# Kernel optimization log

Measured on AMD Instinct MI355X. Metric: run time of the kernel, lower is better.

Reference implementation:

```python
import jax, jax.numpy as jnp
import numpy as np
import math

B, L = 4, 4096
D_MODEL = 1024
D_INNER = 1024          # expand=1
D_STATE = 1             # required by rearrange 'b d 1 l' in ssm()
D_CONV = 2
DT_RANK = 64            # ceil(1024/16)
EPS = 1e-5


def setup_inputs() -> dict:
    key = jax.random.key(0)
    ks = jax.random.split(key, 8)
    dt_min, dt_max, dt_floor = 1e-3, 1e-1, 1e-4
    # dt_proj bias init: inverse-softplus of log-uniform dt (faithful to dt_init)
    dt = jnp.exp(jax.random.uniform(ks[5], (D_INNER,)) * (math.log(dt_max) - math.log(dt_min)) + math.log(dt_min))
    dt = jnp.clip(dt, dt_floor, None)
    inv_dt = dt + jnp.log(-jnp.expm1(-dt))
    std = DT_RANK ** -0.5
    return {
        "x": jax.random.normal(ks[0], (B, L, D_MODEL), dtype=jnp.float32),
        "w_in": jax.random.normal(ks[1], (2 * D_INNER, D_MODEL), dtype=jnp.float32) * 0.02,
        "conv_w": jax.random.normal(ks[2], (D_INNER, 1, D_CONV), dtype=jnp.float32) * 0.5,
        "conv_b": jnp.zeros((D_INNER,), dtype=jnp.float32),
        "x_proj_weight": jax.random.normal(ks[3], (DT_RANK + 2 * D_STATE, D_INNER), dtype=jnp.float32) * 0.02,
        "dt_projs_weight": jax.random.uniform(ks[4], (D_INNER, DT_RANK), minval=-std, maxval=std, dtype=jnp.float32),
        "dt_projs_bias": inv_dt,
        "A_logs": jnp.tile(jnp.log(jnp.arange(1, D_STATE + 1, dtype=jnp.float32))[None, :], (D_INNER, 1)),
        "Ds": jnp.ones((D_INNER,), dtype=jnp.float32),
        "ln_w": jnp.ones((D_INNER,), dtype=jnp.float32),
        "ln_b": jnp.zeros((D_INNER,), dtype=jnp.float32),
        "w_out": jax.random.normal(ks[6], (D_MODEL, D_INNER), dtype=jnp.float32) * 0.02,
    }


def _selective_scan(u, delta, A, Bs):
    # u, delta: (B, D, L); A: (D, N); Bs: (B, N, L) -> hidden states h: (B, D, N, L)
    dA = jnp.exp(jnp.einsum('bdl,dn->bdnl', delta, A))            # (B,D,N,L)
    dBu = jnp.einsum('bdl,bnl,bdl->bdnl', delta, Bs, u)           # delta * B * u
    dA_t = jnp.moveaxis(dA, -1, 0)                                # (L,B,D,N)
    dBu_t = jnp.moveaxis(dBu, -1, 0)

    def step(h, inp):
        a_t, bu_t = inp
        h = a_t * h + bu_t
        return h, h

    h0 = jnp.zeros(dA.shape[:-1], dtype=u.dtype)
    _, hs = jax.lax.scan(step, h0, (dA_t, dBu_t))                 # (L,B,D,N)
    return jnp.moveaxis(hs, 0, -1)                                # (B,D,N,L)


def reference(x, w_in, conv_w, conv_b, x_proj_weight, dt_projs_weight,
              dt_projs_bias, A_logs, Ds, ln_w, ln_b, w_out):
    Bsz, Lsz, _ = x.shape
    # in_proj (bias=False), chunk into x and gate z
    xz = x @ w_in.T                                               # (B,L,2*D)
    xc, z = xz[..., :D_INNER], xz[..., D_INNER:]
    xc = jnp.transpose(xc, (0, 2, 1))                             # (B,D,L)
    # depthwise causal conv1d, padding=d_conv-1, truncated to L
    xc = jax.lax.conv_general_dilated(
        xc, conv_w, window_strides=(1,), padding=[(D_CONV - 1, D_CONV - 1)],
        feature_group_count=D_INNER,
        dimension_numbers=('NCH', 'OIH', 'NCH'))[..., :Lsz]
    xc = xc + conv_b[None, :, None]
    xc = jax.nn.silu(xc)
    # ssm()
    x_dbl = jnp.einsum('rd,bdl->brl', x_proj_weight, xc)          # (B,R+2N,L)
    dts = x_dbl[:, :DT_RANK]
    Bs = x_dbl[:, DT_RANK:DT_RANK + D_STATE]                      # (B,N,L)
    Cs = x_dbl[:, DT_RANK + D_STATE:]                             # (B,N,L)
    dts = jnp.einsum('dr,brl->bdl', dt_projs_weight, dts)         # (B,D,L)
    A = -jnp.exp(A_logs)                                          # (D,N)
    delta = jax.nn.softplus(dts + dt_projs_bias[None, :, None])   # delta_softplus=True
    h = _selective_scan(xc, delta, A, Bs)                         # (B,D,N,L)
    h = h.reshape(Bsz, D_INNER * D_STATE, Lsz)                    # 'b d 1 l -> b (d 1) l' (N==1)
    y = h * Cs + xc * Ds[:, None]                                 # (B,D,L)
    # out_norm (LayerNorm over d_inner), gate, out_proj
    y = jnp.transpose(y, (0, 2, 1))                               # (B,L,D)
    mu = jnp.mean(y, axis=-1, keepdims=True)
    var = jnp.mean(jnp.square(y - mu), axis=-1, keepdims=True)
    y = (y - mu) * jax.lax.rsqrt(var + EPS) * ln_w + ln_b
    y = y * jax.nn.silu(z)
    return y @ w_out.T                                            # (B,L,d_model)
```

## Files before the change

kernel.cpp:

```cpp
#include <hip/hip_runtime.h>
#include <hip/hip_bf16.h>
#include <cstdint>
#include <cstddef>

typedef short short8 __attribute__((ext_vector_type(8)));
typedef short short4v __attribute__((ext_vector_type(4)));
typedef float floatx4 __attribute__((ext_vector_type(4)));

constexpr int Bz = 4;
constexpr int Lz = 4096;
constexpr int Dm = 1024;
constexpr int Di = 1024;
constexpr int Mrows = Bz * Lz;
constexpr int CH  = 128;
constexpr int NCH = Lz / CH;
constexpr int XPJ_KS = 4;

__device__ __forceinline__ void load16(const void* g, void* l) {
  __builtin_amdgcn_global_load_lds((__attribute__((address_space(1))) void*)g,
                                   (__attribute__((address_space(3))) void*)l,
                                   16, 0, 0);
}

__device__ __forceinline__ float bf2f(const __hip_bfloat16 v) { return __bfloat162float(v); }
__device__ __forceinline__ short f2bfs(float v) {
  __hip_bfloat16 h = __float2bfloat16(v);
  return *(short*)&h;
}

__global__ __launch_bounds__(256) void cvt_bf16(const float* __restrict__ in,
                                                __hip_bfloat16* __restrict__ out, int n4)
{
  const int i = blockIdx.x * 256 + threadIdx.x;
  if (i >= n4) return;
  const float4 v = ((const float4*)in)[i];
  short4v s;
  s[0] = f2bfs(v.x); s[1] = f2bfs(v.y); s[2] = f2bfs(v.z); s[3] = f2bfs(v.w);
  ((short4v*)out)[i] = s;
}

__global__ __launch_bounds__(256) void cvt_weights(
    const float* __restrict__ w_in, const float* __restrict__ w_out,
    const float* __restrict__ xpw, const float* __restrict__ dtw,
    __hip_bfloat16* __restrict__ w_in_bf, __hip_bfloat16* __restrict__ w_out_bf,
    __hip_bfloat16* __restrict__ xpw_bf, __hip_bfloat16* __restrict__ dtw_bf)
{
  const int i = blockIdx.x * 256 + threadIdx.x;
  const float* src; __hip_bfloat16* dst; int j;
  if (i < 524288)      { src = w_in;  dst = w_in_bf;  j = i; }
  else if (i < 786432) { src = w_out; dst = w_out_bf; j = i - 524288; }
  else if (i < 803328) { src = xpw;   dst = xpw_bf;   j = i - 786432; }
  else if (i < 819712) { src = dtw;   dst = dtw_bf;   j = i - 803328; }
  else return;
  const float4 v = ((const float4*)src)[j];
  short4v s;
  s[0] = f2bfs(v.x); s[1] = f2bfs(v.y); s[2] = f2bfs(v.z); s[3] = f2bfs(v.w);
  ((short4v*)dst)[j] = s;
}

template <int EPI>
__global__ __launch_bounds__(256) void gemm128(
    const __hip_bfloat16* __restrict__ A,
    const __hip_bfloat16* __restrict__ W,
    int K, int N,
    __hip_bfloat16* __restrict__ outb0,
    __hip_bfloat16* __restrict__ outb1,
    float* __restrict__ outf,
    const float* __restrict__ biasf)
{
  constexpr int BK = 32;
  constexpr int GY = 16;
  __shared__ short sA[128 * BK];
  __shared__ short sB[128 * BK];
  const int tid  = threadIdx.x;
  const int wid  = tid >> 6;
  const int lane = tid & 63;

  const int gx  = gridDim.x;
  const int id  = blockIdx.y * gx + blockIdx.x;
  const int seg = gx * GY;
  const int bx  = (id % seg) / GY;
  const int by  = (id / seg) * GY + (id % GY);

  const int m0 = by * 128;
  const int n0 = bx * 128;
  const int wm = (wid & 1) * 64;
  const int wn = (wid >> 1) * 64;

  floatx4 acc[4][4];
#pragma unroll
  for (int i = 0; i < 4; i++)
#pragma unroll
    for (int j = 0; j < 4; j++) acc[i][j] = (floatx4){0.f, 0.f, 0.f, 0.f};

  const short* Ag = (const short*)A + (size_t)(m0 + (tid >> 2)) * K + (tid & 3) * 8;
  const short* Bg = (const short*)W + (size_t)(n0 + (tid >> 2)) * K + (tid & 3) * 8;
  short* sAd = &sA[tid * 8];
  short* sBd = &sB[tid * 8];
  const size_t rstep = (size_t)64 * K;
  const int fr = lane & 15, fq = lane >> 4;

  for (int kb = 0; kb < K; kb += BK) {
    load16(Ag, sAd);
    load16(Ag + rstep, sAd + 2048);
    load16(Bg, sBd);
    load16(Bg + rstep, sBd + 2048);
    Ag += BK; Bg += BK;
    __syncthreads();

    short8 av[4], bv[4];
#pragma unroll
    for (int mt = 0; mt < 4; mt++) av[mt] = *(const short8*)&sA[(wm + mt * 16 + fr) * BK + fq * 8];
#pragma unroll
    for (int nt = 0; nt < 4; nt++) bv[nt] = *(const short8*)&sB[(wn + nt * 16 + fr) * BK + fq * 8];
#pragma unroll
    for (int mt = 0; mt < 4; mt++)
#pragma unroll
      for (int nt = 0; nt < 4; nt++)
        acc[mt][nt] = __builtin_amdgcn_mfma_f32_16x16x32_bf16(av[mt], bv[nt], acc[mt][nt], 0, 0, 0);
    __syncthreads();
  }

#pragma unroll
  for (int mt = 0; mt < 4; mt++) {
#pragma unroll
    for (int nt = 0; nt < 4; nt++) {
#pragma unroll
      for (int r = 0; r < 4; r++) {
        const int gm = m0 + wm + mt * 16 + fq * 4 + r;
        const int gn = n0 + wn + nt * 16 + fr;
        float v = acc[mt][nt][r];
        if constexpr (EPI == 0) {
          if (gn < 1024) outb0[(size_t)gm * 1024 + gn] = __float2bfloat16(v);
          else           outb1[(size_t)gm * 1024 + (gn - 1024)] = __float2bfloat16(v);
        } else if constexpr (EPI == 1) {
          v += biasf[gn];
          v = (v > 15.f) ? v : __logf(1.f + __expf(v));
          outb0[(size_t)gm * N + gn] = __float2bfloat16(v);
        } else {
          outf[(size_t)gm * N + gn] = v;
        }
      }
    }
  }
}

__device__ __forceinline__ void wait_lgkm0() {
  asm volatile("s_waitcnt lgkmcnt(0)");
  __builtin_amdgcn_sched_barrier(0);
}

template <int EPI>
__device__ __forceinline__ void cluster_mfma(int MQ, floatx4 (&acc)[8][4],
                                             const short8 (&av)[8][2],
                                             const short8 (&bv)[4][2])
{
  __builtin_amdgcn_s_setprio(1);
#pragma unroll
  for (int j = 0; j < 2; j++)
#pragma unroll
    for (int nf = 0; nf < 4; nf++)
#pragma unroll
      for (int ks = 0; ks < 2; ks++)
        acc[2 * MQ + j][nf] = __builtin_amdgcn_mfma_f32_16x16x32_bf16(
            av[2 * MQ + j][ks], bv[nf][ks], acc[2 * MQ + j][nf], 0, 0, 0);
  __builtin_amdgcn_s_setprio(0);
}

template <int EPI>
__global__ __launch_bounds__(512, 2) void gemm256(
    const __hip_bfloat16* __restrict__ A,
    const __hip_bfloat16* __restrict__ W,
    int K, int N,
    __hip_bfloat16* __restrict__ outb0,
    __hip_bfloat16* __restrict__ outb1,
    float* __restrict__ outf)
{
  __shared__ alignas(16) char lds[131072];
  const int tid  = threadIdx.x;
  const int wid  = tid >> 6;
  const int lane = tid & 63;
  const int wm = wid >> 2;
  const int wn = wid & 3;
  const int fr = lane & 15, fq = lane >> 4;

  const int gx   = gridDim.x;
  const int nwg  = gx * gridDim.y;
  const int orig = blockIdx.y * gx + blockIdx.x;
  const int swz  = (orig & 7) * (nwg >> 3) + (orig >> 3);
  const int bx   = swz % gx;
  const int by   = swz / gx;
  const int m0 = by * 256;
  const int n0 = bx * 256;
  const size_t K2 = (size_t)K * 2;

  int rowo[2], colo[2];
#pragma unroll
  for (int i = 0; i < 2; i++) {
    const int p = i * 8192 + tid * 16;
    const int s = p >> 10;
    const int r = (p >> 6) & 15;
    rowo[i] = (s >> 1) * 16 + r;
    colo[i] = (s & 1) * 64 + ((p & 63) ^ (((r >> 3) & 1) << 5));
  }
  const char* Ab = (const char*)A + (size_t)m0 * K2;
  const char* Bb = (const char*)W + (size_t)n0 * K2;
  char* lbase = (char*)lds;

#define STAGE_A(c, h, kt) do {                                                          \
    load16(Ab + (size_t)((h) * 128 + rowo[0]) * K2 + (size_t)(kt) * 128 + colo[0],      \
           lbase + (c) * 32768 + (h) * 16384 + tid * 16);                               \
    load16(Ab + (size_t)((h) * 128 + rowo[1]) * K2 + (size_t)(kt) * 128 + colo[1],      \
           lbase + (c) * 32768 + (h) * 16384 + 8192 + tid * 16);                        \
  } while (0)
#define STAGE_B(c, h, kt) do {                                                          \
    load16(Bb + (size_t)((h) * 128 + rowo[0]) * K2 + (size_t)(kt) * 128 + colo[0],      \
           lbase + 65536 + (c) * 32768 + (h) * 16384 + tid * 16);                       \
    load16(Bb + (size_t)((h) * 128 + rowo[1]) * K2 + (size_t)(kt) * 128 + colo[1],      \
           lbase + 65536 + (c) * 32768 + (h) * 16384 + 8192 + tid * 16);                \
  } while (0)

  const int foff = (fr * 64 + fq * 16) ^ (((fr >> 3) & 1) << 5);

  floatx4 acc[8][4];
#pragma unroll
  for (int i = 0; i < 8; i++)
#pragma unroll
    for (int j = 0; j < 4; j++) acc[i][j] = (floatx4){0.f, 0.f, 0.f, 0.f};

  STAGE_A(0, 0, 0); STAGE_A(0, 1, 0); STAGE_B(0, 0, 0); STAGE_B(0, 1, 0);
  STAGE_B(1, 0, 1); STAGE_B(1, 1, 1); STAGE_A(1, 0, 1);
  asm volatile("s_waitcnt vmcnt(6)");
  __builtin_amdgcn_sched_barrier(0);
  __builtin_amdgcn_s_barrier();

  const int NT = K >> 6;
  short8 av[8][2], bv[4][2];
#pragma unroll 2
  for (int t = 0; t < NT; ++t) {
    const int cur = t & 1, nxt = cur ^ 1;
    const char* la = lbase + cur * 32768 + wm * 16384 + foff;
    const char* lb = lbase + 65536 + cur * 32768 + (wn >> 1) * 16384 + (wn & 1) * 8192 + foff;

#pragma unroll
    for (int nf = 0; nf < 4; nf++)
#pragma unroll
      for (int ks = 0; ks < 2; ks++)
        bv[nf][ks] = *(const short8*)(lb + (nf * 2 + ks) * 1024);
#pragma unroll
    for (int mf = 0; mf < 2; mf++)
#pragma unroll
      for (int ks = 0; ks < 2; ks++)
        av[mf][ks] = *(const short8*)(la + (mf * 2 + ks) * 1024);
    if (t + 1 < NT) STAGE_A(nxt, 1, t + 1);
    __builtin_amdgcn_s_barrier();
    wait_lgkm0();
    cluster_mfma<EPI>(0, acc, av, bv);
    __builtin_amdgcn_s_barrier();

#pragma unroll
    for (int mf = 2; mf < 4; mf++)
#pragma unroll
      for (int ks = 0; ks < 2; ks++)
        av[mf][ks] = *(const short8*)(la + (mf * 2 + ks) * 1024);
    if (t + 2 < NT) STAGE_B(cur, 0, t + 2);
    __builtin_amdgcn_s_barrier();
    wait_lgkm0();
    cluster_mfma<EPI>(1, acc, av, bv);
    __builtin_amdgcn_s_barrier();

#pragma unroll
    for (int mf = 4; mf < 8; mf++)
#pragma unroll
      for (int ks = 0; ks < 2; ks++)
        av[mf][ks] = *(const short8*)(la + (mf * 2 + ks) * 1024);
    if (t + 2 < NT) STAGE_B(cur, 1, t + 2);
    __builtin_amdgcn_s_barrier();
    wait_lgkm0();
    cluster_mfma<EPI>(2, acc, av, bv);
    __builtin_amdgcn_s_barrier();

    if (t + 2 < NT) STAGE_A(cur, 0, t + 2);
    __builtin_amdgcn_s_barrier();
    cluster_mfma<EPI>(3, acc, av, bv);
    if (t < NT - 2) {
      asm volatile("s_waitcnt vmcnt(6)");
      __builtin_amdgcn_sched_barrier(0);
      __builtin_amdgcn_s_barrier();
    } else if (t == NT - 2) {
      asm volatile("s_waitcnt vmcnt(0)");
      __builtin_amdgcn_sched_barrier(0);
      __builtin_amdgcn_s_barrier();
    }
  }
#undef STAGE_A
#undef STAGE_B

#pragma unroll
  for (int mf = 0; mf < 8; mf++) {
#pragma unroll
    for (int nf = 0; nf < 4; nf++) {
#pragma unroll
      for (int r = 0; r < 4; r++) {
        const int gm = m0 + wm * 128 + mf * 16 + fq * 4 + r;
        const int gn = n0 + wn * 64 + nf * 16 + fr;
        const float v = acc[mf][nf][r];
        if constexpr (EPI == 0) {
          if (gn < 1024) outb0[(size_t)gm * 1024 + gn] = __float2bfloat16(v);
          else           outb1[(size_t)gm * 1024 + (gn - 1024)] = __float2bfloat16(v);
        } else {
          outf[(size_t)gm * N + gn] = v;
        }
      }
    }
  }
}

__global__ __launch_bounds__(256) void gemm_xproj(
    const __hip_bfloat16* __restrict__ A,
    const __hip_bfloat16* __restrict__ W,
    float* __restrict__ part)
{
  constexpr int K = 1024, BK = 32, KC = K / XPJ_KS;
  __shared__ short sA[128 * BK];
  __shared__ short sB[80 * BK];
  const int tid = threadIdx.x;
  const int wid = tid >> 6, lane = tid & 63;
  const int kc = blockIdx.x;
  const int m0 = blockIdx.y * 128;

  floatx4 acc[2][5];
#pragma unroll
  for (int i = 0; i < 2; i++)
#pragma unroll
    for (int j = 0; j < 5; j++) acc[i][j] = (floatx4){0.f, 0.f, 0.f, 0.f};

  const short* Ag = (const short*)A + (size_t)(m0 + (tid >> 2)) * K + kc * KC + (tid & 3) * 8;
  const int brow2 = 64 + (tid >> 2);
  const int brow2c = brow2 > 65 ? 65 : brow2;
  const short* Bg  = (const short*)W + (size_t)(tid >> 2) * K + kc * KC + (tid & 3) * 8;
  const short* Bg2 = (const short*)W + (size_t)brow2c * K + kc * KC + (tid & 3) * 8;
  const size_t rstep = (size_t)64 * K;
  const int fr = lane & 15, fq = lane >> 4;

  for (int kb = 0; kb < KC; kb += BK) {
    load16(Ag, &sA[tid * 8]);
    load16(Ag + rstep, &sA[2048 + tid * 8]);
    load16(Bg, &sB[tid * 8]);
    if (tid < 64) load16(Bg2, &sB[2048 + tid * 8]);
    Ag += BK; Bg += BK; Bg2 += BK;
    __syncthreads();

    short8 av[2], bv[5];
#pragma unroll
    for (int mt = 0; mt < 2; mt++) av[mt] = *(const short8*)&sA[(wid * 32 + mt * 16 + fr) * BK + fq * 8];
#pragma unroll
    for (int nt = 0; nt < 5; nt++) bv[nt] = *(const short8*)&sB[(nt * 16 + fr) * BK + fq * 8];
#pragma unroll
    for (int mt = 0; mt < 2; mt++)
#pragma unroll
      for (int nt = 0; nt < 5; nt++)
        acc[mt][nt] = __builtin_amdgcn_mfma_f32_16x16x32_bf16(av[mt], bv[nt], acc[mt][nt], 0, 0, 0);
    __syncthreads();
  }

  float* pp = part + (size_t)kc * Mrows * 66;
#pragma unroll
  for (int mt = 0; mt < 2; mt++) {
#pragma unroll
    for (int nt = 0; nt < 5; nt++) {
#pragma unroll
      for (int r = 0; r < 4; r++) {
        const int gm = m0 + wid * 32 + mt * 16 + fq * 4 + r;
        const int gn = nt * 16 + fr;
        if (gn < 66) pp[(size_t)gm * 66 + gn] = acc[mt][nt][r];
      }
    }
  }
}

__global__ __launch_bounds__(256) void xproj_reduce(
    const float* __restrict__ part,
    __hip_bfloat16* __restrict__ dts,
    float* __restrict__ Bs, float* __restrict__ Cs)
{
  const int i = blockIdx.x * 256 + threadIdx.x;
  if (i >= Mrows * 66) return;
  const int gm = i / 66, gn = i - gm * 66;
  float s = part[i] + part[i + (size_t)Mrows * 66]
          + part[i + (size_t)2 * Mrows * 66] + part[i + (size_t)3 * Mrows * 66];
  if (gn < 64)       dts[(size_t)gm * 64 + gn] = __float2bfloat16(s);
  else if (gn == 64) Bs[gm] = s;
  else               Cs[gm] = s;
}

__global__ __launch_bounds__(256) void conv_silu(
    const __hip_bfloat16* __restrict__ xc, const float* __restrict__ cw,
    const float* __restrict__ cb, __hip_bfloat16* __restrict__ u)
{
  const size_t idx = (size_t)blockIdx.x * 256 + threadIdx.x;
  const int d = (int)(idx & (Di - 1));
  const int l = (int)((idx >> 10) & (Lz - 1));
  const float w0 = cw[2 * d], w1 = cw[2 * d + 1];
  const float prev = (l > 0) ? bf2f(xc[idx - Di]) : 0.f;
  const float v = prev * w0 + bf2f(xc[idx]) * w1 + cb[d];
  const float s = v / (1.f + __expf(-v));
  u[idx] = __float2bfloat16(s);
}

__global__ __launch_bounds__(256) void scan_p1(
    const __hip_bfloat16* __restrict__ delta, const __hip_bfloat16* __restrict__ u,
    const float* __restrict__ Bsv, const float* __restrict__ A_logs,
    float* __restrict__ carryP, float* __restrict__ carryS)
{
  const int d = blockIdx.x * 256 + threadIdx.x;
  const int c = blockIdx.y, b = blockIdx.z;
  const float Ac = -__expf(A_logs[d]);
  size_t base = ((size_t)(b * Lz + c * CH)) * Di + d;
  const float* Bp = Bsv + (size_t)b * Lz + c * CH;
  float P = 1.f, h = 0.f;
#pragma unroll 4
  for (int j = 0; j < CH; j++) {
    const float dl = bf2f(delta[base + (size_t)j * Di]);
    const float uu = bf2f(u[base + (size_t)j * Di]);
    const float a  = __expf(dl * Ac);
    h = a * h + dl * Bp[j] * uu;
    P *= a;
  }
  const int ci = (b * NCH + c) * Di + d;
  carryP[ci] = P;
  carryS[ci] = h;
}

__global__ __launch_bounds__(256) void scan_p2(
    const float* __restrict__ carryP, const float* __restrict__ carryS,
    float* __restrict__ hin)
{
  const int t = blockIdx.x * 256 + threadIdx.x;
  const int b = t >> 10, d = t & (Di - 1);
  float h = 0.f;
  for (int c = 0; c < NCH; c++) {
    const int ci = (b * NCH + c) * Di + d;
    hin[ci] = h;
    h = carryP[ci] * h + carryS[ci];
  }
}

__global__ __launch_bounds__(256) void scan_p3(
    const __hip_bfloat16* __restrict__ delta, __hip_bfloat16* __restrict__ uy,
    const float* __restrict__ Bsv, const float* __restrict__ Csv,
    const float* __restrict__ A_logs, const float* __restrict__ Ds,
    const float* __restrict__ hin)
{
  const int d = blockIdx.x * 256 + threadIdx.x;
  const int c = blockIdx.y, b = blockIdx.z;
  const float Ac = -__expf(A_logs[d]);
  const float Dd = Ds[d];
  size_t base = ((size_t)(b * Lz + c * CH)) * Di + d;
  const float* Bp = Bsv + (size_t)b * Lz + c * CH;
  const float* Cp = Csv + (size_t)b * Lz + c * CH;
  float h = hin[(b * NCH + c) * Di + d];
#pragma unroll 4
  for (int j = 0; j < CH; j++) {
    const size_t ix = base + (size_t)j * Di;
    const float dl = bf2f(delta[ix]);
    const float uu = bf2f(uy[ix]);
    const float a  = __expf(dl * Ac);
    h = a * h + dl * Bp[j] * uu;
    uy[ix] = __float2bfloat16(h * Cp[j] + uu * Dd);
  }
}

__global__ __launch_bounds__(256) void ln_gate(
    const __hip_bfloat16* __restrict__ y, const __hip_bfloat16* __restrict__ z,
    const float* __restrict__ lnw, const float* __restrict__ lnb,
    __hip_bfloat16* __restrict__ yg)
{
  const int row = blockIdx.x;
  const int tid = threadIdx.x;
  const int wid = tid >> 6, lane = tid & 63;
  const short4v yv = *(const short4v*)((const short*)y + (size_t)row * Di + tid * 4);
  float v[4];
#pragma unroll
  for (int i = 0; i < 4; i++) {
    __hip_bfloat16 t;
    *(short*)&t = yv[i];
    v[i] = bf2f(t);
  }
  float s1 = v[0] + v[1] + v[2] + v[3];
  float s2 = v[0] * v[0] + v[1] * v[1] + v[2] * v[2] + v[3] * v[3];
#pragma unroll
  for (int o = 32; o > 0; o >>= 1) {
    s1 += __shfl_down(s1, o, 64);
    s2 += __shfl_down(s2, o, 64);
  }
  __shared__ float r1[4], r2[4];
  if (lane == 0) { r1[wid] = s1; r2[wid] = s2; }
  __syncthreads();
  const float t1 = r1[0] + r1[1] + r1[2] + r1[3];
  const float t2 = r2[0] + r2[1] + r2[2] + r2[3];
  const float mu = t1 * (1.f / Di);
  const float var = t2 * (1.f / Di) - mu * mu;
  const float rstd = rsqrtf(var + 1e-5f);

  const float4 wv = ((const float4*)lnw)[tid];
  const float4 bv = ((const float4*)lnb)[tid];
  const float wa[4] = {wv.x, wv.y, wv.z, wv.w};
  const float ba[4] = {bv.x, bv.y, bv.z, bv.w};
  const __hip_bfloat16* zr = z + (size_t)row * Di + tid * 4;
  __hip_bfloat16* outp = yg + (size_t)row * Di + tid * 4;
#pragma unroll
  for (int i = 0; i < 4; i++) {
    const float zv = bf2f(zr[i]);
    const float g = zv / (1.f + __expf(-zv));
    outp[i] = __float2bfloat16(((v[i] - mu) * rstd * wa[i] + ba[i]) * g);
  }
}

__global__ __launch_bounds__(256) void fill_diag(float* __restrict__ out, int n, float val)
{
  const int i = blockIdx.x * 256 + threadIdx.x;
  if (i < n) out[i] = val;
}

extern "C" void kernel_launch(void* const* d_in, const int* in_sizes, int n_in,
                              void* d_out, int out_size, void* d_ws, size_t ws_size,
                              hipStream_t stream)
{
  const float* x      = (const float*)d_in[0];
  const float* w_in   = (const float*)d_in[1];
  const float* conv_w = (const float*)d_in[2];
  const float* conv_b = (const float*)d_in[3];
  const float* xpw    = (const float*)d_in[4];
  const float* dtw    = (const float*)d_in[5];
  const float* dtb    = (const float*)d_in[6];
  const float* A_logs = (const float*)d_in[7];
  const float* Ds     = (const float*)d_in[8];
  const float* lnw    = (const float*)d_in[9];
  const float* lnb    = (const float*)d_in[10];
  const float* w_out  = (const float*)d_in[11];
  float* outF = (float*)d_out;

  const size_t BF16BIG  = (size_t)Mrows * Di * sizeof(__hip_bfloat16);
  const size_t NEED_RUN = 69603328;

  if (ws_size < NEED_RUN) {
    fill_diag<<<(out_size + 255) / 256, 256, 0, stream>>>(
        outF, out_size, (float)(ws_size >> 10));
    return;
  }

  uint8_t* ws = (uint8_t*)d_ws;
  size_t off = 0;
  auto alloc = [&](size_t bytes) { void* p = ws + off; off += (bytes + 255) & ~(size_t)255; return p; };

  __hip_bfloat16* slotA    = (__hip_bfloat16*)alloc(BF16BIG);
  __hip_bfloat16* slotC    = (__hip_bfloat16*)alloc(BF16BIG);
  __hip_bfloat16* w_out_bf = (__hip_bfloat16*)alloc((size_t)Dm * Di * 2);
  __hip_bfloat16* xpw_bf   = (__hip_bfloat16*)alloc((size_t)66 * Di * 2);
  __hip_bfloat16* dtw_bf   = (__hip_bfloat16*)alloc((size_t)Di * 64 * 2);
  float* Bsv = (float*)alloc((size_t)Mrows * sizeof(float));
  float* Csv = (float*)alloc((size_t)Mrows * sizeof(float));

  __hip_bfloat16* zbuf    = (__hip_bfloat16*)d_out;
  __hip_bfloat16* w_in_bf = (__hip_bfloat16*)((uint8_t*)d_out + 33554432);
  uint8_t* dts_region     = (uint8_t*)d_out + 37748736;
  float* xpj_part         = (float*)((uint8_t*)d_out + 41943040);
  __hip_bfloat16* dts = (__hip_bfloat16*)dts_region;
  float* carryP = (float*)dts_region;
  float* carryS = carryP + (size_t)Bz * NCH * Di;
  float* hin    = carryS + (size_t)Bz * NCH * Di;

  __hip_bfloat16* xbf   = slotC;
  __hip_bfloat16* xcbuf = slotA;
  __hip_bfloat16* ubuf  = slotC;
  __hip_bfloat16* delta = slotA;
  __hip_bfloat16* yg    = slotA;

  cvt_bf16<<<(Mrows * Di / 4 + 255) / 256, 256, 0, stream>>>(x, xbf, Mrows * Di / 4);
  cvt_weights<<<(819712 + 255) / 256, 256, 0, stream>>>(
      w_in, w_out, xpw, dtw, w_in_bf, w_out_bf, xpw_bf, dtw_bf);

  gemm256<0><<<dim3(2 * Di / 256, Mrows / 256), 512, 0, stream>>>(
      xbf, w_in_bf, Dm, 2 * Di, xcbuf, zbuf, nullptr);
  conv_silu<<<(Mrows * Di) / 256, 256, 0, stream>>>(xcbuf, conv_w, conv_b, ubuf);
  gemm_xproj<<<dim3(XPJ_KS, Mrows / 128), 256, 0, stream>>>(ubuf, xpw_bf, xpj_part);
  xproj_reduce<<<(Mrows * 66 + 255) / 256, 256, 0, stream>>>(xpj_part, dts, Bsv, Csv);
  gemm128<1><<<dim3(Di / 128, Mrows / 128), 256, 0, stream>>>(
      dts, dtw_bf, 64, Di, delta, nullptr, nullptr, dtb);
  scan_p1<<<dim3(Di / 256, NCH, Bz), 256, 0, stream>>>(delta, ubuf, Bsv, A_logs, carryP, carryS);
  scan_p2<<<(Bz * Di) / 256, 256, 0, stream>>>(carryP, carryS, hin);
  scan_p3<<<dim3(Di / 256, NCH, Bz), 256, 0, stream>>>(delta, ubuf, Bsv, Csv, A_logs, Ds, hin);
  ln_gate<<<Mrows, 256, 0, stream>>>(ubuf, zbuf, lnw, lnb, yg);
  gemm256<1><<<dim3(Dm / 256, Mrows / 256), 512, 0, stream>>>(
      yg, w_out_bf, Di, Dm, nullptr, nullptr, outF);
}
```

Before: 365.7 us.

## Shorten scan chunks, process channel pairs, vectorize conv and LN, merge conversions

Reduces the scan chunk length so the chunked scan exposes more blocks, and has each thread handle two adjacent channels using packed bf16 loads and stores. The conv+SiLU and LayerNorm-gate kernels now use 8- and 4-wide vector memory accesses, and the input and weight bf16 conversions merge into one launch. The carry buffers are repositioned in scratch to fit the larger chunk count. This adds more carry traffic and a longer sequential pass in scan_p2, which is now spread over smaller blocks.

```diff
diff --git a/kernel.cpp b/kernel.cpp
--- a/kernel.cpp
+++ b/kernel.cpp
@@ -12,7 +12,7 @@
 constexpr int Dm = 1024;
 constexpr int Di = 1024;
 constexpr int Mrows = Bz * Lz;
-constexpr int CH  = 128;
+constexpr int CH  = 32;
 constexpr int NCH = Lz / CH;
 constexpr int XPJ_KS = 4;
 
@@ -28,29 +28,21 @@
   return *(short*)&h;
 }
 
-__global__ __launch_bounds__(256) void cvt_bf16(const float* __restrict__ in,
-                                                __hip_bfloat16* __restrict__ out, int n4)
-{
-  const int i = blockIdx.x * 256 + threadIdx.x;
-  if (i >= n4) return;
-  const float4 v = ((const float4*)in)[i];
-  short4v s;
-  s[0] = f2bfs(v.x); s[1] = f2bfs(v.y); s[2] = f2bfs(v.z); s[3] = f2bfs(v.w);
-  ((short4v*)out)[i] = s;
-}
-
-__global__ __launch_bounds__(256) void cvt_weights(
-    const float* __restrict__ w_in, const float* __restrict__ w_out,
-    const float* __restrict__ xpw, const float* __restrict__ dtw,
-    __hip_bfloat16* __restrict__ w_in_bf, __hip_bfloat16* __restrict__ w_out_bf,
-    __hip_bfloat16* __restrict__ xpw_bf, __hip_bfloat16* __restrict__ dtw_bf)
+__global__ __launch_bounds__(256) void cvt_all(
+    const float* __restrict__ x, const float* __restrict__ w_in,
+    const float* __restrict__ w_out, const float* __restrict__ xpw,
+    const float* __restrict__ dtw,
+    __hip_bfloat16* __restrict__ xbf, __hip_bfloat16* __restrict__ w_in_bf,
+    __hip_bfloat16* __restrict__ w_out_bf, __hip_bfloat16* __restrict__ xpw_bf,
+    __hip_bfloat16* __restrict__ dtw_bf)
 {
   const int i = blockIdx.x * 256 + threadIdx.x;
   const float* src; __hip_bfloat16* dst; int j;
-  if (i < 524288)      { src = w_in;  dst = w_in_bf;  j = i; }
-  else if (i < 786432) { src = w_out; dst = w_out_bf; j = i - 524288; }
-  else if (i < 803328) { src = xpw;   dst = xpw_bf;   j = i - 786432; }
-  else if (i < 819712) { src = dtw;   dst = dtw_bf;   j = i - 803328; }
+  if (i < 4194304)      { src = x;     dst = xbf;      j = i; }
+  else if (i < 4718592) { src = w_in;  dst = w_in_bf;  j = i - 4194304; }
+  else if (i < 4980736) { src = w_out; dst = w_out_bf; j = i - 4718592; }
+  else if (i < 4997632) { src = xpw;   dst = xpw_bf;   j = i - 4980736; }
+  else if (i < 5014016) { src = dtw;   dst = dtw_bf;   j = i - 4997632; }
   else return;
   const float4 v = ((const float4*)src)[j];
   short4v s;
@@ -398,14 +390,30 @@
     const __hip_bfloat16* __restrict__ xc, const float* __restrict__ cw,
     const float* __restrict__ cb, __hip_bfloat16* __restrict__ u)
 {
-  const size_t idx = (size_t)blockIdx.x * 256 + threadIdx.x;
-  const int d = (int)(idx & (Di - 1));
-  const int l = (int)((idx >> 10) & (Lz - 1));
-  const float w0 = cw[2 * d], w1 = cw[2 * d + 1];
-  const float prev = (l > 0) ? bf2f(xc[idx - Di]) : 0.f;
-  const float v = prev * w0 + bf2f(xc[idx]) * w1 + cb[d];
-  const float s = v / (1.f + __expf(-v));
-  u[idx] = __float2bfloat16(s);
+  const size_t i8 = ((size_t)blockIdx.x * 256 + threadIdx.x) * 8;
+  const int d8 = (int)(i8 & (Di - 1));
+  const int l  = (int)((i8 >> 10) & (Lz - 1));
+  const short8 cur = *(const short8*)((const short*)xc + i8);
+  short8 prv;
+  if (l > 0) prv = *(const short8*)((const short*)xc + i8 - Di);
+  else       prv = (short8){0, 0, 0, 0, 0, 0, 0, 0};
+  const float4* cw4 = (const float4*)(cw + 2 * d8);
+  const float4 wA = cw4[0], wB = cw4[1], wC = cw4[2], wD = cw4[3];
+  const float w0a[8] = {wA.x, wA.z, wB.x, wB.z, wC.x, wC.z, wD.x, wD.z};
+  const float w1a[8] = {wA.y, wA.w, wB.y, wB.w, wC.y, wC.w, wD.y, wD.w};
+  const float4* cb4 = (const float4*)(cb + d8);
+  const float4 b0 = cb4[0], b1 = cb4[1];
+  const float ba[8] = {b0.x, b0.y, b0.z, b0.w, b1.x, b1.y, b1.z, b1.w};
+  short8 out;
+#pragma unroll
+  for (int k = 0; k < 8; k++) {
+    const float pc = __uint_as_float(((uint32_t)(uint16_t)prv[k]) << 16);
+    const float cc = __uint_as_float(((uint32_t)(uint16_t)cur[k]) << 16);
+    const float v = pc * w0a[k] + cc * w1a[k] + ba[k];
+    const float s = v / (1.f + __expf(-v));
+    out[k] = f2bfs(s);
+  }
+  *(short8*)((short*)u + i8) = out;
 }
 
 __global__ __launch_bounds__(256) void scan_p1(
@@ -413,34 +421,42 @@
     const float* __restrict__ Bsv, const float* __restrict__ A_logs,
     float* __restrict__ carryP, float* __restrict__ carryS)
 {
-  const int d = blockIdx.x * 256 + threadIdx.x;
+  const int dp = blockIdx.x * 256 + threadIdx.x;
+  const int d  = dp * 2;
   const int c = blockIdx.y, b = blockIdx.z;
-  const float Ac = -__expf(A_logs[d]);
-  size_t base = ((size_t)(b * Lz + c * CH)) * Di + d;
+  const float2 Al = *(const float2*)(A_logs + d);
+  const float Ac0 = -__expf(Al.x), Ac1 = -__expf(Al.y);
+  const size_t base = ((size_t)(b * Lz + c * CH)) * Di + d;
   const float* Bp = Bsv + (size_t)b * Lz + c * CH;
-  float P = 1.f, h = 0.f;
-#pragma unroll 4
+  float P0 = 1.f, h0 = 0.f, P1 = 1.f, h1 = 0.f;
+#pragma unroll 8
   for (int j = 0; j < CH; j++) {
-    const float dl = bf2f(delta[base + (size_t)j * Di]);
-    const float uu = bf2f(u[base + (size_t)j * Di]);
-    const float a  = __expf(dl * Ac);
-    h = a * h + dl * Bp[j] * uu;
-    P *= a;
-  }
-  const int ci = (b * NCH + c) * Di + d;
-  carryP[ci] = P;
-  carryS[ci] = h;
-}
-
-__global__ __launch_bounds__(256) void scan_p2(
+    const uint32_t dv = *(const uint32_t*)((const uint16_t*)delta + base + (size_t)j * Di);
+    const uint32_t uv = *(const uint32_t*)((const uint16_t*)u + base + (size_t)j * Di);
+    const float dl0 = __uint_as_float(dv << 16);
+    const float dl1 = __uint_as_float(dv & 0xffff0000u);
+    const float uu0 = __uint_as_float(uv << 16);
+    const float uu1 = __uint_as_float(uv & 0xffff0000u);
+    const float bj  = Bp[j];
+    const float a0 = __expf(dl0 * Ac0), a1 = __expf(dl1 * Ac1);
+    h0 = a0 * h0 + dl0 * bj * uu0;
+    h1 = a1 * h1 + dl1 * bj * uu1;
+    P0 *= a0; P1 *= a1;
+  }
+  const size_t ci = ((size_t)(b * NCH + c)) * Di + d;
+  *(float2*)(carryP + ci) = make_float2(P0, P1);
+  *(float2*)(carryS + ci) = make_float2(h0, h1);
+}
+
+__global__ __launch_bounds__(64) void scan_p2(
     const float* __restrict__ carryP, const float* __restrict__ carryS,
     float* __restrict__ hin)
 {
-  const int t = blockIdx.x * 256 + threadIdx.x;
+  const int t = blockIdx.x * 64 + threadIdx.x;
   const int b = t >> 10, d = t & (Di - 1);
   float h = 0.f;
   for (int c = 0; c < NCH; c++) {
-    const int ci = (b * NCH + c) * Di + d;
+    const size_t ci = ((size_t)(b * NCH + c)) * Di + d;
     hin[ci] = h;
     h = carryP[ci] * h + carryS[ci];
   }
@@ -452,22 +468,35 @@
     const float* __restrict__ A_logs, const float* __restrict__ Ds,
     const float* __restrict__ hin)
 {
-  const int d = blockIdx.x * 256 + threadIdx.x;
+  const int dp = blockIdx.x * 256 + threadIdx.x;
+  const int d  = dp * 2;
   const int c = blockIdx.y, b = blockIdx.z;
-  const float Ac = -__expf(A_logs[d]);
-  const float Dd = Ds[d];
-  size_t base = ((size_t)(b * Lz + c * CH)) * Di + d;
+  const float2 Al = *(const float2*)(A_logs + d);
+  const float Ac0 = -__expf(Al.x), Ac1 = -__expf(Al.y);
+  const float2 Dd = *(const float2*)(Ds + d);
+  const size_t base = ((size_t)(b * Lz + c * CH)) * Di + d;
   const float* Bp = Bsv + (size_t)b * Lz + c * CH;
   const float* Cp = Csv + (size_t)b * Lz + c * CH;
-  float h = hin[(b * NCH + c) * Di + d];
-#pragma unroll 4
+  const size_t ci = ((size_t)(b * NCH + c)) * Di + d;
+  const float2 hh = *(const float2*)(hin + ci);
+  float h0 = hh.x, h1 = hh.y;
+#pragma unroll 8
   for (int j = 0; j < CH; j++) {
     const size_t ix = base + (size_t)j * Di;
-    const float dl = bf2f(delta[ix]);
-    const float uu = bf2f(uy[ix]);
-    const float a  = __expf(dl * Ac);
-    h = a * h + dl * Bp[j] * uu;
-    uy[ix] = __float2bfloat16(h * Cp[j] + uu * Dd);
+    const uint32_t dv = *(const uint32_t*)((const uint16_t*)delta + ix);
+    const uint32_t uv = *(const uint32_t*)((const uint16_t*)uy + ix);
+    const float dl0 = __uint_as_float(dv << 16);
+    const float dl1 = __uint_as_float(dv & 0xffff0000u);
+    const float uu0 = __uint_as_float(uv << 16);
+    const float uu1 = __uint_as_float(uv & 0xffff0000u);
+    const float bj = Bp[j], cj = Cp[j];
+    const float a0 = __expf(dl0 * Ac0), a1 = __expf(dl1 * Ac1);
+    h0 = a0 * h0 + dl0 * bj * uu0;
+    h1 = a1 * h1 + dl1 * bj * uu1;
+    const float y0 = h0 * cj + uu0 * Dd.x;
+    const float y1 = h1 * cj + uu1 * Dd.y;
+    const uint32_t o = (uint32_t)(uint16_t)f2bfs(y0) | ((uint32_t)(uint16_t)f2bfs(y1) << 16);
+    *(uint32_t*)((uint16_t*)uy + ix) = o;
   }
 }
 
@@ -480,13 +509,11 @@
   const int tid = threadIdx.x;
   const int wid = tid >> 6, lane = tid & 63;
   const short4v yv = *(const short4v*)((const short*)y + (size_t)row * Di + tid * 4);
+  const short4v zv4 = *(const short4v*)((const short*)z + (size_t)row * Di + tid * 4);
   float v[4];
 #pragma unroll
-  for (int i = 0; i < 4; i++) {
-    __hip_bfloat16 t;
-    *(short*)&t = yv[i];
-    v[i] = bf2f(t);
-  }
+  for (int i = 0; i < 4; i++)
+    v[i] = __uint_as_float(((uint32_t)(uint16_t)yv[i]) << 16);
   float s1 = v[0] + v[1] + v[2] + v[3];
   float s2 = v[0] * v[0] + v[1] * v[1] + v[2] * v[2] + v[3] * v[3];
 #pragma unroll
@@ -507,14 +534,14 @@
   const float4 bv = ((const float4*)lnb)[tid];
   const float wa[4] = {wv.x, wv.y, wv.z, wv.w};
   const float ba[4] = {bv.x, bv.y, bv.z, bv.w};
-  const __hip_bfloat16* zr = z + (size_t)row * Di + tid * 4;
-  __hip_bfloat16* outp = yg + (size_t)row * Di + tid * 4;
+  short4v og;
 #pragma unroll
   for (int i = 0; i < 4; i++) {
-    const float zv = bf2f(zr[i]);
-    const float g = zv / (1.f + __expf(-zv));
-    outp[i] = __float2bfloat16(((v[i] - mu) * rstd * wa[i] + ba[i]) * g);
-  }
+    const float zz = __uint_as_float(((uint32_t)(uint16_t)zv4[i]) << 16);
+    const float g = zz / (1.f + __expf(-zz));
+    og[i] = f2bfs(((v[i] - mu) * rstd * wa[i] + ba[i]) * g);
+  }
+  *(short4v*)((short*)yg + (size_t)row * Di + tid * 4) = og;
 }
 
 __global__ __launch_bounds__(256) void fill_diag(float* __restrict__ out, int n, float val)
@@ -564,12 +591,11 @@
 
   __hip_bfloat16* zbuf    = (__hip_bfloat16*)d_out;
   __hip_bfloat16* w_in_bf = (__hip_bfloat16*)((uint8_t*)d_out + 33554432);
-  uint8_t* dts_region     = (uint8_t*)d_out + 37748736;
-  float* xpj_part         = (float*)((uint8_t*)d_out + 41943040);
-  __hip_bfloat16* dts = (__hip_bfloat16*)dts_region;
-  float* carryP = (float*)dts_region;
-  float* carryS = carryP + (size_t)Bz * NCH * Di;
-  float* hin    = carryS + (size_t)Bz * NCH * Di;
+  __hip_bfloat16* dts     = (__hip_bfloat16*)((uint8_t*)d_out + 37748736);
+  float* carryP = (float*)((uint8_t*)d_out + 39845888);
+  float* carryS = (float*)((uint8_t*)d_out + 41943040);
+  float* hin    = (float*)((uint8_t*)d_out + 44040192);
+  float* xpj_part = (float*)((uint8_t*)d_out + 41943040);
 
   __hip_bfloat16* xbf   = slotC;
   __hip_bfloat16* xcbuf = slotA;
@@ -577,20 +603,19 @@
   __hip_bfloat16* delta = slotA;
   __hip_bfloat16* yg    = slotA;
 
-  cvt_bf16<<<(Mrows * Di / 4 + 255) / 256, 256, 0, stream>>>(x, xbf, Mrows * Di / 4);
-  cvt_weights<<<(819712 + 255) / 256, 256, 0, stream>>>(
-      w_in, w_out, xpw, dtw, w_in_bf, w_out_bf, xpw_bf, dtw_bf);
+  cvt_all<<<(5014016 + 255) / 256, 256, 0, stream>>>(
+      x, w_in, w_out, xpw, dtw, xbf, w_in_bf, w_out_bf, xpw_bf, dtw_bf);
 
   gemm256<0><<<dim3(2 * Di / 256, Mrows / 256), 512, 0, stream>>>(
       xbf, w_in_bf, Dm, 2 * Di, xcbuf, zbuf, nullptr);
-  conv_silu<<<(Mrows * Di) / 256, 256, 0, stream>>>(xcbuf, conv_w, conv_b, ubuf);
+  conv_silu<<<(Mrows * Di / 8) / 256, 256, 0, stream>>>(xcbuf, conv_w, conv_b, ubuf);
   gemm_xproj<<<dim3(XPJ_KS, Mrows / 128), 256, 0, stream>>>(ubuf, xpw_bf, xpj_part);
   xproj_reduce<<<(Mrows * 66 + 255) / 256, 256, 0, stream>>>(xpj_part, dts, Bsv, Csv);
   gemm128<1><<<dim3(Di / 128, Mrows / 128), 256, 0, stream>>>(
       dts, dtw_bf, 64, Di, delta, nullptr, nullptr, dtb);
-  scan_p1<<<dim3(Di / 256, NCH, Bz), 256, 0, stream>>>(delta, ubuf, Bsv, A_logs, carryP, carryS);
-  scan_p2<<<(Bz * Di) / 256, 256, 0, stream>>>(carryP, carryS, hin);
-  scan_p3<<<dim3(Di / 256, NCH, Bz), 256, 0, stream>>>(delta, ubuf, Bsv, Csv, A_logs, Ds, hin);
+  scan_p1<<<dim3(Di / 512, NCH, Bz), 256, 0, stream>>>(delta, ubuf, Bsv, A_logs, carryP, carryS);
+  scan_p2<<<(Bz * Di) / 64, 64, 0, stream>>>(carryP, carryS, hin);
+  scan_p3<<<dim3(Di / 512, NCH, Bz), 256, 0, stream>>>(delta, ubuf, Bsv, Csv, A_logs, Ds, hin);
   ln_gate<<<Mrows, 256, 0, stream>>>(ubuf, zbuf, lnw, lnb, yg);
   gemm256<1><<<dim3(Dm / 256, Mrows / 256), 512, 0, stream>>>(
       yg, w_out_bf, Di, Dm, nullptr, nullptr, outF);
```

Result: faster. 353.6 us (-3.3%).
